# Kernel optimization log

Measured on AMD Instinct MI355X. Metric: run time of the kernel, lower is better.

Reference implementation:

```python
import jax, jax.numpy as jnp
import numpy as np

# e3nn normalize2mom gain for tanh (1/sqrt(E[tanh(z)^2]), z~N(0,1))
TANH_GAIN = 1.5927116870880127
B, M_IN, M_HID, M_OUT = 8192, 64, 128, 64

_W_SPECS = {
    'b1_l1_w0': (64, 64), 'b1_l1_w1': (64, 64), 'b1_l2_w0': (64, 64), 'b1_l2_w1': (64, 64),
    'b1_tp_ss': (64, 64, 128), 'b1_tp_vv': (64, 64, 128), 'b1_tp_sv': (64, 64, 128), 'b1_tp_vs': (64, 64, 128),
    'b1_g_ws': (128, 128), 'b1_g_wg': (128, 128), 'b1_g_wv': (128, 128),
    'b1_o_w0': (128, 128), 'b1_o_w1': (128, 128),
    'b2_l1_w0': (128, 128), 'b2_l1_w1': (128, 128), 'b2_l2_w0': (128, 128), 'b2_l2_w1': (128, 128),
    'b2_tp_ss': (128, 128, 128), 'b2_tp_vv': (128, 128, 128), 'b2_tp_sv': (128, 128, 128), 'b2_tp_vs': (128, 128, 128),
    'b2_g_ws': (128, 128), 'b2_g_wg': (128, 128), 'b2_g_wv': (128, 128),
    'b2_o_w0': (128, 128), 'b2_o_w1': (128, 128),
    'f_w0': (128, 64), 'f_w1': (128, 64),
}


def setup_inputs() -> dict:
    key = jax.random.key(0)
    ks = jax.random.split(key, len(_W_SPECS) + 1)
    d = {'x': jax.random.normal(ks[0], (B, M_IN + 3 * M_IN), jnp.float32)}
    for i, (name, shp) in enumerate(_W_SPECS.items()):
        d[name] = jax.random.normal(ks[i + 1], shp, jnp.float32)  # e3nn weights ~ N(0,1)
    return d


def _lin(s, v, w0, w1):
    # o3.Linear on 'Mx0e+Mx1o': per-irrep block matmul, path_normalization='element' -> 1/sqrt(fan_in)
    c = 1.0 / np.sqrt(w0.shape[0])
    return (s @ w0) * c, jnp.einsum('bui,uw->bwi', v, w1) * c


def _tp(s1, v1, s2, v2, wss, wvv, wsv, wvs):
    # FullyConnectedTensorProduct, irrep_normalization='component', path_normalization='element'.
    # Two uvw paths feed each output irrep -> path_weight = sqrt(dim_out / (2*M*M)).
    # CG values: w3j(0,0,0)=1; w3j(0,1,1)=delta/sqrt(3); w3j(1,0,1)=delta/sqrt(3); w3j(1,1,0)=delta/sqrt(3).
    M = s1.shape[-1]
    c = 1.0 / (M * np.sqrt(2.0))
    s = c * jnp.einsum('bu,bv,uvw->bw', s1, s2, wss) \
        + (c / np.sqrt(3.0)) * jnp.einsum('bui,bvi,uvw->bw', v1, v2, wvv)
    v = c * (jnp.einsum('bu,bvi,uvw->bwi', s1, v2, wsv)
             + jnp.einsum('bui,bv,uvw->bwi', v1, s2, wvs))
    return s, v


def _gate(s, v, ws, wg, wv):
    # LearnableGate: o3.Linear to (scalars | gate scalars | vectors), then e3nn Gate
    # (tanh w/ normalize2mom gain on scalars and gates; elementwise gate*vector has unit path weight).
    c = 1.0 / np.sqrt(ws.shape[0])
    sl = (s @ ws) * c
    g = (s @ wg) * c
    vl = jnp.einsum('bui,uw->bwi', v, wv) * c
    return TANH_GAIN * jnp.tanh(sl), (TANH_GAIN * jnp.tanh(g))[..., None] * vl


def _block(s, v, p):
    l1w0, l1w1, l2w0, l2w1, wss, wvv, wsv, wvs, gws, gwg, gwv, ow0, ow1 = p
    s1, v1 = _lin(s, v, l1w0, l1w1)
    s2, v2 = _lin(s, v, l2w0, l2w1)
    s, v = _tp(s1, v1, s2, v2, wss, wvv, wsv, wvs)
    s, v = _gate(s, v, gws, gwg, gwv)
    return _lin(s, v, ow0, ow1)


def _forward(x, *w):
    s = x[:, :M_IN]
    v = x[:, M_IN:].reshape(x.shape[0], M_IN, 3)
    s, v = _block(s, v, w[0:13])
    s, v = _block(s, v, w[13:26])
    s, v = _lin(s, v, w[26], w[27])
    return jnp.concatenate([s, v.reshape(v.shape[0], -1)], axis=-1)


def reference(x, b1_l1_w0, b1_l1_w1, b1_l2_w0, b1_l2_w1, b1_tp_ss, b1_tp_vv, b1_tp_sv, b1_tp_vs, b1_g_ws, b1_g_wg, b1_g_wv, b1_o_w0, b1_o_w1, b2_l1_w0, b2_l1_w1, b2_l2_w0, b2_l2_w1, b2_tp_ss, b2_tp_vv, b2_tp_sv, b2_tp_vs, b2_g_ws, b2_g_wg, b2_g_wv, b2_o_w0, b2_o_w1, f_w0, f_w1):
    return _forward(x, b1_l1_w0, b1_l1_w1, b1_l2_w0, b1_l2_w1, b1_tp_ss, b1_tp_vv, b1_tp_sv, b1_tp_vs, b1_g_ws, b1_g_wg, b1_g_wv, b1_o_w0, b1_o_w1, b2_l1_w0, b2_l1_w1, b2_l2_w0, b2_l2_w1, b2_tp_ss, b2_tp_vv, b2_tp_sv, b2_tp_vs, b2_g_ws, b2_g_wg, b2_g_wv, b2_o_w0, b2_o_w1, f_w0, f_w1)
```

## Files before the change

kernel.cpp:

```cpp
#include <hip/hip_runtime.h>
#include <math.h>

typedef _Float16 f16;
typedef __attribute__((ext_vector_type(8))) _Float16 half8;
typedef __attribute__((ext_vector_type(4))) _Float16 half4;
typedef __attribute__((ext_vector_type(4))) float floatx4;

#define NB 8192

struct ConvJob { const float* src; f16* dst; int K; int N; int ucount; float scale; int swz; };
struct ConvJobs { ConvJob j[28]; };

__global__ void convert_w(ConvJobs JJ) {
    ConvJob jb = JJ.j[blockIdx.z];
    int u = blockIdx.x;
    if (u >= jb.ucount) return;
    __shared__ f16 tile[128 * 136];
    const int K = jb.K, N = jb.N;
    const int npad = N + 8;
    const int nsh = (N == 128) ? 7 : 6;
    const int ksh = (K == 128) ? 7 : 6;
    const float* src = jb.src + (size_t)u * K * N;
    for (int idx = threadIdx.x; idx < K * N; idx += 256) {
        int k = idx >> nsh, n = idx & (N - 1);
        tile[k * npad + n] = (f16)(src[idx] * jb.scale);
    }
    __syncthreads();
    f16* dst = jb.dst + (size_t)u * N * K;
    for (int idx = threadIdx.x; idx < N * K; idx += 256) {
        int n = idx >> ksh, rem = idx & (K - 1);
        int g2 = rem >> 3, jj = rem & 7;
        int g = jb.swz ? (g2 ^ (n & jb.swz)) : g2;
        int k = g * 8 + jj;
        dst[idx] = tile[k * npad + n];
    }
}

__global__ void x_to_planes(const float* __restrict__ x, f16* s_p, f16* v0, f16* v1, f16* v2) {
    int t = blockIdx.x * 256 + threadIdx.x;
    if (t >= NB * 64) return;
    int b = t >> 6, u = t & 63;
    const float* xr = x + (size_t)b * 256;
    s_p[t] = (f16)xr[u];
    v0[t] = (f16)xr[64 + 3 * u + 0];
    v1[t] = (f16)xr[64 + 3 * u + 1];
    v2[t] = (f16)xr[64 + 3 * u + 2];
}

struct TpJob { const f16* p; const f16* q; const f16* w; float* out; int pstride; int qstride; };
struct TpJobs { TpJob j[10]; };

template <int M>
__launch_bounds__(256, (M == 128) ? 3 : 4)
__global__ void tp_unit(TpJobs JJ) {
    TpJob jb = JJ.j[blockIdx.z];
    constexpr int KC = M / 32;
    constexpr int GM = M / 8 - 1;
    constexpr int SLABH = 64 * M;
    constexpr int PIECES = SLABH / 8;
    constexpr int IPW = PIECES / 256;
    constexpr int SLABFULL = 128 * M;
    __shared__ f16 w_lds[3][SLABH];
    const int tid = threadIdx.x, lane = tid & 63, wave = tid >> 6;
    const int wm = wave & 1, wn = wave >> 1;
    const int l15 = lane & 15, quad = lane >> 4;
    const int rowBase = blockIdx.x * 128;
    const int colBase = blockIdx.y * 64;

    half8 qf[4][KC];
    int prow[4];
    #pragma unroll
    for (int t = 0; t < 4; t++) {
        int row = rowBase + wm * 64 + t * 16 + l15;
        prow[t] = row;
        const f16* qr = jb.q + (size_t)row * jb.qstride;
        #pragma unroll
        for (int c = 0; c < KC; c++) qf[t][c] = *(const half8*)(qr + c * 32 + quad * 8);
    }
    floatx4 acc[4][2];
    #pragma unroll
    for (int a = 0; a < 4; a++)
        #pragma unroll
        for (int b = 0; b < 2; b++) acc[a][b] = (floatx4){0.f, 0.f, 0.f, 0.f};

    int rd_off[2][KC];
    #pragma unroll
    for (int nt = 0; nt < 2; nt++) {
        int nl = wn * 32 + nt * 16 + l15;
        #pragma unroll
        for (int c = 0; c < KC; c++) {
            int g = c * 4 + quad;
            rd_off[nt][c] = nl * M + ((g ^ (nl & GM)) << 3);
        }
    }

    const int wpBase = wave * (PIECES / 4);
    const f16* wsrc0 = jb.w + (size_t)colBase * M + (size_t)(wpBase + lane) * 8;
    auto stage = [&](int u, int buf) {
        const f16* src = wsrc0 + (size_t)u * SLABFULL;
        f16* dst = &w_lds[buf][0] + (size_t)wpBase * 8;
        #pragma unroll
        for (int i = 0; i < IPW; i++) {
            __builtin_amdgcn_global_load_lds(
                (const __attribute__((address_space(1))) void*)(src + i * 64 * 8),
                (__attribute__((address_space(3))) void*)(dst + i * 64 * 8),
                16, 0, 0);
        }
    };

    stage(0, 0);
    stage(1, 1);

    int sl = 0;
    for (int uc = 0; uc < M / 8; uc++) {
        half8 pcur[4];
        #pragma unroll
        for (int t = 0; t < 4; t++)
            pcur[t] = *(const half8*)(jb.p + (size_t)prow[t] * jb.pstride + uc * 8);
        #pragma unroll
        for (int j = 0; j < 8; j++) {
            const int u = uc * 8 + j;
            if (u == M - 1) asm volatile("s_waitcnt vmcnt(0)" ::: "memory");
            else            asm volatile("s_waitcnt vmcnt(%0)" :: "n"(IPW) : "memory");
            __builtin_amdgcn_s_barrier();
            asm volatile("" ::: "memory");
            if (u < M - 2) {
                int st = sl - 1; if (st < 0) st = 2;
                stage(u + 2, st);
            }
            const f16* wl = &w_lds[sl][0];
            #pragma unroll
            for (int c = 0; c < KC; c++) {
                half8 af[4];
                #pragma unroll
                for (int t = 0; t < 4; t++) {
                    f16 pv = pcur[t][j];
                    half8 p8 = {pv, pv, pv, pv, pv, pv, pv, pv};
                    af[t] = qf[t][c] * p8;
                }
                __builtin_amdgcn_s_setprio(1);
                #pragma unroll
                for (int nt = 0; nt < 2; nt++) {
                    half8 bf = *(const half8*)(wl + rd_off[nt][c]);
                    #pragma unroll
                    for (int t = 0; t < 4; t++)
                        acc[t][nt] = __builtin_amdgcn_mfma_f32_16x16x32_f16(af[t], bf, acc[t][nt], 0, 0, 0);
                }
                __builtin_amdgcn_s_setprio(0);
            }
            sl = (sl == 2) ? 0 : sl + 1;
        }
    }
    #pragma unroll
    for (int t = 0; t < 4; t++)
        #pragma unroll
        for (int nt = 0; nt < 2; nt++) {
            int col = colBase + wn * 32 + nt * 16 + l15;
            float* orow = jb.out + (size_t)(rowBase + wm * 64 + t * 16 + quad * 4) * 128 + col;
            #pragma unroll
            for (int r = 0; r < 4; r++) orow[(size_t)r * 128] = acc[t][nt][r];
        }
}

struct SmallJob { const f16* A; const f16* W; char* out; int astride; int ostride;
                  int ocol; int cstride; int mode; int Njob; int ny;
                  const f16* Amul; int mstride;
                  const float* red0; const float* red1; const float* red2; const float* red3;
                  int nred; };
struct SmallJobs { SmallJob j[4]; };

template <int K>
__launch_bounds__(256, 2)
__global__ void small_gemm(SmallJobs JJ) {
    SmallJob jb = JJ.j[blockIdx.z];
    if ((int)blockIdx.y >= jb.ny) return;
    constexpr int KC = K / 32;
    constexpr int NP = K + 8;
    constexpr int PR = K / 8;
    constexpr int PPT = 128 * K / 8 / 256;
    __shared__ f16 w_lds[128 * NP];
    const int tid = threadIdx.x, lane = tid & 63, wave = tid >> 6;
    const int wm = wave & 1, wn = wave >> 1;
    const int l15 = lane & 15, quad = lane >> 4;
    const int rowBase = blockIdx.x * 64;
    const int nBase = blockIdx.y * 128;

    #pragma unroll
    for (int t = 0; t < PPT; t++) {
        int idx = t * 256 + tid;
        int r = idx / PR, pc = idx % PR;
        int4 v = {0, 0, 0, 0};
        if (nBase + r < jb.Njob)
            v = *(const int4*)(jb.W + (size_t)(nBase + r) * K + pc * 8);
        *(int4*)&w_lds[r * NP + pc * 8] = v;
    }
    half8 qf[2][KC];
    for (int t = 0; t < 2; t++) {
        int row = rowBase + wm * 32 + t * 16 + l15;
        if (jb.nred) {
            #pragma unroll
            for (int c = 0; c < KC; c++) {
                size_t boff = (size_t)row * 128 + c * 32 + quad * 8;
                floatx4 s0 = *(const floatx4*)(jb.red0 + boff);
                floatx4 s1 = *(const floatx4*)(jb.red0 + boff + 4);
                if (jb.nred > 1) { s0 += *(const floatx4*)(jb.red1 + boff); s1 += *(const floatx4*)(jb.red1 + boff + 4); }
                if (jb.nred > 2) { s0 += *(const floatx4*)(jb.red2 + boff); s1 += *(const floatx4*)(jb.red2 + boff + 4); }
                if (jb.nred > 3) { s0 += *(const floatx4*)(jb.red3 + boff); s1 += *(const floatx4*)(jb.red3 + boff + 4); }
                qf[t][c] = (half8){(f16)s0.x, (f16)s0.y, (f16)s0.z, (f16)s0.w,
                                   (f16)s1.x, (f16)s1.y, (f16)s1.z, (f16)s1.w};
            }
        } else {
            const f16* ar = jb.A + (size_t)row * jb.astride;
            #pragma unroll
            for (int c = 0; c < KC; c++) qf[t][c] = *(const half8*)(ar + c * 32 + quad * 8);
        }
        if (jb.Amul) {
            const f16* mr = jb.Amul + (size_t)row * jb.mstride;
            #pragma unroll
            for (int c = 0; c < KC; c++) qf[t][c] = qf[t][c] * *(const half8*)(mr + c * 32 + quad * 8);
        }
    }
    floatx4 acc[2][4];
    #pragma unroll
    for (int a = 0; a < 2; a++)
        #pragma unroll
        for (int b = 0; b < 4; b++) acc[a][b] = (floatx4){0.f, 0.f, 0.f, 0.f};
    __syncthreads();
    #pragma unroll
    for (int c = 0; c < KC; c++)
        #pragma unroll
        for (int nt = 0; nt < 4; nt++) {
            half8 bf = *(const half8*)&w_lds[(wn * 64 + nt * 16 + l15) * NP + c * 32 + quad * 8];
            #pragma unroll
            for (int t = 0; t < 2; t++)
                acc[t][nt] = __builtin_amdgcn_mfma_f32_16x16x32_f16(qf[t][c], bf, acc[t][nt], 0, 0, 0);
        }
    const float GAIN = 1.5927116870880127f;
    #pragma unroll
    for (int t = 0; t < 2; t++)
        #pragma unroll
        for (int nt = 0; nt < 4; nt++) {
            int col = nBase + wn * 64 + nt * 16 + l15;
            if (col >= jb.Njob) continue;
            int rowB = rowBase + wm * 32 + t * 16 + quad * 4;
            #pragma unroll
            for (int r = 0; r < 4; r++) {
                float v = acc[t][nt][r];
                size_t ro = (size_t)(rowB + r) * jb.ostride;
                if (jb.mode == 0)      ((f16*)jb.out)[ro + jb.ocol + col] = (f16)v;
                else if (jb.mode == 1) ((f16*)jb.out)[ro + jb.ocol + col] = (f16)(GAIN * tanhf(v));
                else                   ((float*)jb.out)[ro + jb.ocol + (size_t)col * jb.cstride] = v;
            }
        }
}

extern "C" void kernel_launch(void* const* d_in, const int* in_sizes, int n_in,
                              void* d_out, int out_size, void* d_ws, size_t ws_size,
                              hipStream_t stream) {
    const float* x = (const float*)d_in[0];
    const float* W_IN[28];
    for (int i = 0; i < 28; i++) W_IN[i] = (const float*)d_in[1 + i];

    char* base = (char*)d_ws;
    size_t off = 0;
    auto alloc = [&](size_t bytes) -> char* {
        char* p = base + off;
        off += (bytes + 255) & ~(size_t)255;
        return p;
    };
    const size_t S128 = (size_t)NB * 128;

    f16* Wl12_b1_s = (f16*)alloc(8192 * 2);
    f16* Wl12_b1_v = (f16*)alloc(8192 * 2);
    f16* Wl12_b2_s = (f16*)alloc(32768 * 2);
    f16* Wl12_b2_v = (f16*)alloc(32768 * 2);
    f16* Wtp_b1[4]; for (int i = 0; i < 4; i++) Wtp_b1[i] = (f16*)alloc((size_t)64 * 128 * 64 * 2);
    f16* Wtp_b2[4]; for (int i = 0; i < 4; i++) Wtp_b2[i] = (f16*)alloc((size_t)128 * 128 * 128 * 2);
    f16* Wg_b1_sg = (f16*)alloc(32768 * 2);
    f16* Wg_b1_v  = (f16*)alloc(16384 * 2);
    f16* Wg_b2_sg = (f16*)alloc(32768 * 2);
    f16* Wg_b2_v  = (f16*)alloc(16384 * 2);
    f16* Wo_b1_s = (f16*)alloc(16384 * 2);
    f16* Wo_b1_v = (f16*)alloc(16384 * 2);
    f16* Wo_b2_s = (f16*)alloc(16384 * 2);
    f16* Wo_b2_v = (f16*)alloc(16384 * 2);
    f16* Wf_s = (f16*)alloc(8192 * 2);
    f16* Wf_v = (f16*)alloc(8192 * 2);
    f16* s_p = (f16*)alloc((size_t)NB * 64 * 2);
    f16* v_p[3]; for (int i = 0; i < 3; i++) v_p[i] = (f16*)alloc((size_t)NB * 64 * 2);
    f16* Breg = (f16*)alloc((size_t)4 * NB * 256 * 2);
    float* Part = (float*)alloc((size_t)10 * S128 * 4);
    f16* Ereg = (f16*)alloc((size_t)5 * S128 * 2);
    f16* Freg = (f16*)alloc((size_t)4 * S128 * 2);
    (void)ws_size; (void)in_sizes; (void)n_in; (void)out_size;

    const float c_l1 = 0.125f;
    const float c128 = 0.088388347648318447f;
    const float c1 = 1.0f / (64.0f * 1.4142135623730951f);
    const float c2 = 1.0f / (128.0f * 1.4142135623730951f);
    const float i3 = 0.57735026918962584f;

    ConvJobs CJ;
    int jn = 0;
    auto CV = [&](const float* s, f16* d, int K, int N, int uc, float sc, int swz) {
        CJ.j[jn++] = ConvJob{s, d, K, N, uc, sc, swz};
    };
    CV(W_IN[0], Wl12_b1_s, 64, 64, 1, c_l1, 0);  CV(W_IN[2], Wl12_b1_s + 4096, 64, 64, 1, c_l1, 0);
    CV(W_IN[1], Wl12_b1_v, 64, 64, 1, c_l1, 0);  CV(W_IN[3], Wl12_b1_v + 4096, 64, 64, 1, c_l1, 0);
    CV(W_IN[13], Wl12_b2_s, 128, 128, 1, c128, 0); CV(W_IN[15], Wl12_b2_s + 16384, 128, 128, 1, c128, 0);
    CV(W_IN[14], Wl12_b2_v, 128, 128, 1, c128, 0); CV(W_IN[16], Wl12_b2_v + 16384, 128, 128, 1, c128, 0);
    CV(W_IN[4], Wtp_b1[0], 64, 128, 64, c1, 7);  CV(W_IN[5], Wtp_b1[1], 64, 128, 64, c1 * i3, 7);
    CV(W_IN[6], Wtp_b1[2], 64, 128, 64, c1, 7);  CV(W_IN[7], Wtp_b1[3], 64, 128, 64, c1, 7);
    CV(W_IN[17], Wtp_b2[0], 128, 128, 128, c2, 15); CV(W_IN[18], Wtp_b2[1], 128, 128, 128, c2 * i3, 15);
    CV(W_IN[19], Wtp_b2[2], 128, 128, 128, c2, 15); CV(W_IN[20], Wtp_b2[3], 128, 128, 128, c2, 15);
    CV(W_IN[8], Wg_b1_sg, 128, 128, 1, c128, 0);  CV(W_IN[9], Wg_b1_sg + 16384, 128, 128, 1, c128, 0);
    CV(W_IN[10], Wg_b1_v, 128, 128, 1, c128, 0);
    CV(W_IN[21], Wg_b2_sg, 128, 128, 1, c128, 0); CV(W_IN[22], Wg_b2_sg + 16384, 128, 128, 1, c128, 0);
    CV(W_IN[23], Wg_b2_v, 128, 128, 1, c128, 0);
    CV(W_IN[11], Wo_b1_s, 128, 128, 1, c128, 0);  CV(W_IN[12], Wo_b1_v, 128, 128, 1, c128, 0);
    CV(W_IN[24], Wo_b2_s, 128, 128, 1, c128, 0);  CV(W_IN[25], Wo_b2_v, 128, 128, 1, c128, 0);
    CV(W_IN[26], Wf_s, 128, 64, 1, c128, 0);      CV(W_IN[27], Wf_v, 128, 64, 1, c128, 0);
    convert_w<<<dim3(128, 1, 28), 256, 0, stream>>>(CJ);

    x_to_planes<<<NB * 64 / 256, 256, 0, stream>>>(x, s_p, v_p[0], v_p[1], v_p[2]);

    auto SJ = [](const f16* A, const f16* W, void* out, int as, int os, int oc, int cs,
                 int mode, int Nj, int ny, const f16* Amul, int ms) {
        return SmallJob{A, W, (char*)out, as, os, oc, cs, mode, Nj, ny, Amul, ms,
                        nullptr, nullptr, nullptr, nullptr, 0};
    };

    f16* s12 = Breg;
    f16* v12[3]; for (int i = 0; i < 3; i++) v12[i] = Breg + (size_t)(1 + i) * NB * 128;
    f16* sg_gg = Ereg;
    f16* vl[3]; for (int i = 0; i < 3; i++) vl[i] = Ereg + 2 * S128 + i * S128;
    f16* s_o = Freg; f16* v_o[3]; for (int i = 0; i < 3; i++) v_o[i] = Freg + (1 + i) * S128;

    {
        SmallJobs J;
        J.j[0] = SJ(s_p, Wl12_b1_s, s12, 64, 128, 0, 1, 0, 128, 1, nullptr, 0);
        for (int i = 0; i < 3; i++) J.j[1 + i] = SJ(v_p[i], Wl12_b1_v, v12[i], 64, 128, 0, 1, 0, 128, 1, nullptr, 0);
        small_gemm<64><<<dim3(128, 1, 4), 256, 0, stream>>>(J);
    }
    {
        TpJobs J;
        J.j[0] = TpJob{s12, s12 + 64, Wtp_b1[0], Part + 0 * S128, 128, 128};
        for (int i = 0; i < 3; i++) J.j[1 + i] = TpJob{v12[i], v12[i] + 64, Wtp_b1[1], Part + (1 + i) * S128, 128, 128};
        for (int i = 0; i < 3; i++) J.j[4 + i] = TpJob{s12, v12[i] + 64, Wtp_b1[2], Part + (4 + i) * S128, 128, 128};
        for (int i = 0; i < 3; i++) J.j[7 + i] = TpJob{v12[i], s12 + 64, Wtp_b1[3], Part + (7 + i) * S128, 128, 128};
        tp_unit<64><<<dim3(64, 2, 10), 256, 0, stream>>>(J);
    }
    {
        SmallJobs J;
        J.j[0] = SmallJob{nullptr, Wg_b1_sg, (char*)sg_gg, 128, 256, 0, 1, 1, 256, 2, nullptr, 0,
                          Part + 0 * S128, Part + 1 * S128, Part + 2 * S128, Part + 3 * S128, 4};
        for (int i = 0; i < 3; i++)
            J.j[1 + i] = SmallJob{nullptr, Wg_b1_v, (char*)vl[i], 128, 128, 0, 1, 0, 128, 1, nullptr, 0,
                                  Part + (4 + i) * S128, Part + (7 + i) * S128, nullptr, nullptr, 2};
        small_gemm<128><<<dim3(128, 2, 4), 256, 0, stream>>>(J);
    }
    {
        SmallJobs J;
        J.j[0] = SJ(sg_gg, Wo_b1_s, s_o, 256, 128, 0, 1, 0, 128, 1, nullptr, 0);
        for (int i = 0; i < 3; i++) J.j[1 + i] = SJ(vl[i], Wo_b1_v, v_o[i], 128, 128, 0, 1, 0, 128, 1, sg_gg + 128, 256);
        small_gemm<128><<<dim3(128, 1, 4), 256, 0, stream>>>(J);
    }
    f16* s12b = Breg;
    f16* v12b[3]; for (int i = 0; i < 3; i++) v12b[i] = Breg + (size_t)(1 + i) * NB * 256;
    {
        SmallJobs J;
        J.j[0] = SJ(s_o, Wl12_b2_s, s12b, 128, 256, 0, 1, 0, 256, 2, nullptr, 0);
        for (int i = 0; i < 3; i++) J.j[1 + i] = SJ(v_o[i], Wl12_b2_v, v12b[i], 128, 256, 0, 1, 0, 256, 2, nullptr, 0);
        small_gemm<128><<<dim3(128, 2, 4), 256, 0, stream>>>(J);
    }
    {
        TpJobs J;
        J.j[0] = TpJob{s12b, s12b + 128, Wtp_b2[0], Part + 0 * S128, 256, 256};
        for (int i = 0; i < 3; i++) J.j[1 + i] = TpJob{v12b[i], v12b[i] + 128, Wtp_b2[1], Part + (1 + i) * S128, 256, 256};
        for (int i = 0; i < 3; i++) J.j[4 + i] = TpJob{s12b, v12b[i] + 128, Wtp_b2[2], Part + (4 + i) * S128, 256, 256};
        for (int i = 0; i < 3; i++) J.j[7 + i] = TpJob{v12b[i], s12b + 128, Wtp_b2[3], Part + (7 + i) * S128, 256, 256};
        tp_unit<128><<<dim3(64, 2, 10), 256, 0, stream>>>(J);
    }
    {
        SmallJobs J;
        J.j[0] = SmallJob{nullptr, Wg_b2_sg, (char*)sg_gg, 128, 256, 0, 1, 1, 256, 2, nullptr, 0,
                          Part + 0 * S128, Part + 1 * S128, Part + 2 * S128, Part + 3 * S128, 4};
        for (int i = 0; i < 3; i++)
            J.j[1 + i] = SmallJob{nullptr, Wg_b2_v, (char*)vl[i], 128, 128, 0, 1, 0, 128, 1, nullptr, 0,
                                  Part + (4 + i) * S128, Part + (7 + i) * S128, nullptr, nullptr, 2};
        small_gemm<128><<<dim3(128, 2, 4), 256, 0, stream>>>(J);
    }
    {
        SmallJobs J;
        J.j[0] = SJ(sg_gg, Wo_b2_s, s_o, 256, 128, 0, 1, 0, 128, 1, nullptr, 0);
        for (int i = 0; i < 3; i++) J.j[1 + i] = SJ(vl[i], Wo_b2_v, v_o[i], 128, 128, 0, 1, 0, 128, 1, sg_gg + 128, 256);
        small_gemm<128><<<dim3(128, 1, 4), 256, 0, stream>>>(J);
    }
    {
        SmallJobs J;
        J.j[0] = SJ(s_o, Wf_s, d_out, 128, 256, 0, 1, 2, 64, 1, nullptr, 0);
        for (int i = 0; i < 3; i++) J.j[1 + i] = SJ(v_o[i], Wf_v, d_out, 128, 256, 64 + i, 3, 2, 64, 1, nullptr, 0);
        small_gemm<128><<<dim3(128, 1, 4), 256, 0, stream>>>(J);
    }
}
```

Before: 645.8 us.

## Switch tensor-product kernel to 32x32x16 MFMA and stagger u-slab start per block

Replaces the 16x16x32 MFMA tiling in tp_unit with 32x32x16 MFMA, so each wave holds 2 row tiles of 32 instead of 4x2 tiles of 16. This halves the LDS B-fragment reads per A element and cuts the number of MFMA instructions. It also rotates the starting u-chunk per block so concurrent blocks read different weight slabs, spreading cache and channel pressure. The costs are a different register layout and a more complex output store pattern.

```diff
diff --git a/kernel.cpp b/kernel.cpp
--- a/kernel.cpp
+++ b/kernel.cpp
@@ -3,8 +3,8 @@
 
 typedef _Float16 f16;
 typedef __attribute__((ext_vector_type(8))) _Float16 half8;
-typedef __attribute__((ext_vector_type(4))) _Float16 half4;
 typedef __attribute__((ext_vector_type(4))) float floatx4;
+typedef __attribute__((ext_vector_type(16))) float floatx16;
 
 #define NB 8192
 
@@ -54,43 +54,43 @@
 __launch_bounds__(256, (M == 128) ? 3 : 4)
 __global__ void tp_unit(TpJobs JJ) {
     TpJob jb = JJ.j[blockIdx.z];
-    constexpr int KC = M / 32;
+    constexpr int KC = M / 16;
     constexpr int GM = M / 8 - 1;
     constexpr int SLABH = 64 * M;
     constexpr int PIECES = SLABH / 8;
     constexpr int IPW = PIECES / 256;
     constexpr int SLABFULL = 128 * M;
+    constexpr int UCN = M / 8;
     __shared__ f16 w_lds[3][SLABH];
     const int tid = threadIdx.x, lane = tid & 63, wave = tid >> 6;
     const int wm = wave & 1, wn = wave >> 1;
-    const int l15 = lane & 15, quad = lane >> 4;
+    const int l31 = lane & 31, khalf = lane >> 5;
     const int rowBase = blockIdx.x * 128;
     const int colBase = blockIdx.y * 64;
 
-    half8 qf[4][KC];
-    int prow[4];
-    #pragma unroll
-    for (int t = 0; t < 4; t++) {
-        int row = rowBase + wm * 64 + t * 16 + l15;
+    half8 qf[2][KC];
+    int prow[2];
+    #pragma unroll
+    for (int t = 0; t < 2; t++) {
+        int row = rowBase + wm * 64 + t * 32 + l31;
         prow[t] = row;
         const f16* qr = jb.q + (size_t)row * jb.qstride;
         #pragma unroll
-        for (int c = 0; c < KC; c++) qf[t][c] = *(const half8*)(qr + c * 32 + quad * 8);
-    }
-    floatx4 acc[4][2];
-    #pragma unroll
-    for (int a = 0; a < 4; a++)
-        #pragma unroll
-        for (int b = 0; b < 2; b++) acc[a][b] = (floatx4){0.f, 0.f, 0.f, 0.f};
-
-    int rd_off[2][KC];
-    #pragma unroll
-    for (int nt = 0; nt < 2; nt++) {
-        int nl = wn * 32 + nt * 16 + l15;
+        for (int c = 0; c < KC; c++) qf[t][c] = *(const half8*)(qr + c * 16 + khalf * 8);
+    }
+    floatx16 acc[2];
+    #pragma unroll
+    for (int t = 0; t < 2; t++)
+        #pragma unroll
+        for (int r = 0; r < 16; r++) acc[t][r] = 0.f;
+
+    int rd_off[KC];
+    {
+        int nl = wn * 32 + l31;
         #pragma unroll
         for (int c = 0; c < KC; c++) {
-            int g = c * 4 + quad;
-            rd_off[nt][c] = nl * M + ((g ^ (nl & GM)) << 3);
+            int g = c * 2 + khalf;
+            rd_off[c] = nl * M + ((g ^ (nl & GM)) << 3);
         }
     }
 
@@ -108,58 +108,58 @@
         }
     };
 
-    stage(0, 0);
-    stage(1, 1);
+    const int uc0 = (int)((blockIdx.x * 5u + blockIdx.y * 3u + blockIdx.z) % (unsigned)UCN);
+    auto uphys = [&](int i) { int u = uc0 * 8 + i; return (u >= M) ? u - M : u; };
+
+    stage(uphys(0), 0);
+    stage(uphys(1), 1);
 
     int sl = 0;
-    for (int uc = 0; uc < M / 8; uc++) {
-        half8 pcur[4];
-        #pragma unroll
-        for (int t = 0; t < 4; t++)
-            pcur[t] = *(const half8*)(jb.p + (size_t)prow[t] * jb.pstride + uc * 8);
+    for (int ic = 0; ic < UCN; ic++) {
+        int ucp = uc0 + ic; if (ucp >= UCN) ucp -= UCN;
+        half8 pcur[2];
+        #pragma unroll
+        for (int t = 0; t < 2; t++)
+            pcur[t] = *(const half8*)(jb.p + (size_t)prow[t] * jb.pstride + ucp * 8);
         #pragma unroll
         for (int j = 0; j < 8; j++) {
-            const int u = uc * 8 + j;
-            if (u == M - 1) asm volatile("s_waitcnt vmcnt(0)" ::: "memory");
+            const int i = ic * 8 + j;
+            if (i == M - 1) asm volatile("s_waitcnt vmcnt(0)" ::: "memory");
             else            asm volatile("s_waitcnt vmcnt(%0)" :: "n"(IPW) : "memory");
             __builtin_amdgcn_s_barrier();
             asm volatile("" ::: "memory");
-            if (u < M - 2) {
+            if (i < M - 2) {
                 int st = sl - 1; if (st < 0) st = 2;
-                stage(u + 2, st);
+                stage(uphys(i + 2), st);
             }
             const f16* wl = &w_lds[sl][0];
+            __builtin_amdgcn_s_setprio(1);
             #pragma unroll
             for (int c = 0; c < KC; c++) {
-                half8 af[4];
+                half8 bf = *(const half8*)(wl + rd_off[c]);
                 #pragma unroll
-                for (int t = 0; t < 4; t++) {
+                for (int t = 0; t < 2; t++) {
                     f16 pv = pcur[t][j];
                     half8 p8 = {pv, pv, pv, pv, pv, pv, pv, pv};
-                    af[t] = qf[t][c] * p8;
+                    half8 af = qf[t][c] * p8;
+                    acc[t] = __builtin_amdgcn_mfma_f32_32x32x16_f16(af, bf, acc[t], 0, 0, 0);
                 }
-                __builtin_amdgcn_s_setprio(1);
-                #pragma unroll
-                for (int nt = 0; nt < 2; nt++) {
-                    half8 bf = *(const half8*)(wl + rd_off[nt][c]);
-                    #pragma unroll
-                    for (int t = 0; t < 4; t++)
-                        acc[t][nt] = __builtin_amdgcn_mfma_f32_16x16x32_f16(af[t], bf, acc[t][nt], 0, 0, 0);
-                }
-                __builtin_amdgcn_s_setprio(0);
             }
+            __builtin_amdgcn_s_setprio(0);
             sl = (sl == 2) ? 0 : sl + 1;
         }
     }
     #pragma unroll
-    for (int t = 0; t < 4; t++)
-        #pragma unroll
-        for (int nt = 0; nt < 2; nt++) {
-            int col = colBase + wn * 32 + nt * 16 + l15;
-            float* orow = jb.out + (size_t)(rowBase + wm * 64 + t * 16 + quad * 4) * 128 + col;
-            #pragma unroll
-            for (int r = 0; r < 4; r++) orow[(size_t)r * 128] = acc[t][nt][r];
-        }
+    for (int t = 0; t < 2; t++) {
+        int col = colBase + wn * 32 + l31;
+        int rbase = rowBase + wm * 64 + t * 32 + 4 * khalf;
+        float* o = jb.out + (size_t)rbase * 128 + col;
+        #pragma unroll
+        for (int r = 0; r < 16; r++) {
+            int row_off = (r & 3) + 8 * (r >> 2);
+            o[(size_t)row_off * 128] = acc[t][r];
+        }
+    }
 }
 
 struct SmallJob { const f16* A; const f16* W; char* out; int astride; int ostride;
```

New measurement: 669.8 us. 3.7% more time.
